# Kernel optimization log

Hardware: AMD Instinct MI355X
Metric: run time of the kernel (lower is better)

The kernel has to match this reference:

```python
import jax, jax.numpy as jnp
import numpy as np

N = 1200        # nodes in the (complete) graph
SLOPE = 0.1     # leaky_relu negative slope
# smat: 10-vector -> symmetric 4x4
SMAT_IDX = np.array([0,1,2,3,1,4,5,6,2,5,7,8,3,6,8,9])

def _glorot(k, shape):
    lim = float(np.sqrt(6.0 / (shape[0] + shape[1])))
    return jax.random.uniform(k, shape, jnp.float32, -lim, lim)

def setup_inputs():
    key = jax.random.key(0)
    ks = jax.random.split(key, 24)
    # complete graph connectivity (recover_S reads edge_map[i,j] for all i!=j)
    iu, ju = np.triu_indices(N, k=1)
    E = iu.shape[0]
    eid = np.arange(E, dtype=np.int32)
    edge_map = np.zeros((N, N), dtype=np.int32)
    edge_map[iu, ju] = eid
    edge_map[ju, iu] = eid
    ud_edges = np.stack([iu, ju], axis=1).astype(np.int32)           # [E,2]
    edge_index = np.stack([np.concatenate([iu, ju]),
                           np.concatenate([ju, iu])]).astype(np.int32)  # [2,2E]
    inp = {
        'x': jax.random.normal(ks[0], (N, 16), jnp.float32),
        'edge_index': jnp.asarray(edge_index),
        'edge_map': jnp.asarray(edge_map),
        'ud_edges': jnp.asarray(ud_edges),
    }
    dims = {'g': [(6, 32), (32, 32), (32, 64)],
            'n': [(64, 64), (64, 64), (64, 10)],
            'e': [(64, 64), (64, 64), (64, 16)]}
    k = 1
    for tag, ds in dims.items():
        for i, (a, b) in enumerate(ds):
            inp[f'W{tag}{i+1}'] = _glorot(ks[k], (a, b)); k += 1
            inp[f'b{tag}{i+1}'] = jnp.zeros((b,), jnp.float32)
    return inp

def _leaky(v):
    return jnp.where(v >= 0, v, SLOPE * v)

def _gcn(x, src, dst, W, b):
    deg = jax.ops.segment_sum(jnp.ones(src.shape[0], x.dtype), dst, num_segments=N)
    dinv = jnp.where(deg > 0, jax.lax.rsqrt(deg), 0.0)
    norm = dinv[src] * dinv[dst]
    h = x @ W
    return jax.ops.segment_sum(norm[:, None] * h[src], dst, num_segments=N) + b

def _mlp3(h, W1, b1, W2, b2, W3, b3):
    # dropout is identity (eval mode)
    h = _leaky(h @ W1 + b1)
    h = _leaky(h @ W2 + b2)
    return h @ W3 + b3

def _forward(x, edge_index, edge_map, ud_edges,
             Wg1, bg1, Wg2, bg2, Wg3, bg3,
             Wn1, bn1, Wn2, bn2, Wn3, bn3,
             We1, be1, We2, be2, We3, be3):
    x6 = x[:, 0:6]                       # node_feature_mode == 1
    src, dst = edge_index[0], edge_index[1]
    h = _leaky(_gcn(x6, src, dst, Wg1, bg1))
    h = _leaky(_gcn(h, src, dst, Wg2, bg2))
    h = _gcn(h, src, dst, Wg3, bg3)      # [N,64]
    vd = _mlp3(h, Wn1, bn1, Wn2, bn2, Wn3, bn3)            # [N,10]
    he = h[ud_edges[:, 0]] + h[ud_edges[:, 1]]             # [E,64]
    ed = _mlp3(he, We1, be1, We2, be2, We3, be3)           # [E,16]
    # recover_S: block-structured [4N,4N]
    Vsym = vd[:, jnp.asarray(SMAT_IDX)].reshape(N, 4, 4)   # smat per node
    Eb = ed.reshape(-1, 4, 4)
    B = Eb[edge_map]                                       # [N,N,4,4]
    ii = jnp.arange(N)
    lower = ii[:, None] > ii[None, :]
    B = jnp.where(lower[:, :, None, None], jnp.swapaxes(B, 2, 3), B)
    B = B.at[ii, ii].set(Vsym)
    S = B.transpose(0, 2, 1, 3).reshape(4 * N, 4 * N)
    return h, S

def reference(x, edge_index, edge_map, ud_edges,
              Wg1, bg1, Wg2, bg2, Wg3, bg3,
              Wn1, bn1, Wn2, bn2, Wn3, bn3,
              We1, be1, We2, be2, We3, be3):
    return _forward(x, edge_index, edge_map, ud_edges,
                    Wg1, bg1, Wg2, bg2, Wg3, bg3,
                    Wn1, bn1, Wn2, bn2, Wn3, bn3,
                    We1, be1, We2, be2, We3, be3)
```

## Files before the change

kernel.cpp:

```cpp
#include <hip/hip_runtime.h>

#define NN 1200
#define NE 719400
#define SDIM 4800

typedef __attribute__((ext_vector_type(8))) short bf16x8;
typedef __attribute__((ext_vector_type(4))) short bf16x4;
typedef __attribute__((ext_vector_type(4))) float f32x4;

static __device__ __constant__ int SMAT[16] = {0,1,2,3,1,4,5,6,2,5,7,8,3,6,8,9};

__device__ __forceinline__ float lk(float v) { return v >= 0.f ? v : 0.1f * v; }

#if __has_builtin(__builtin_amdgcn_mfma_f32_16x16x16bf16_1k)
__device__ __forceinline__ f32x4 mfma1616(bf16x4 a, bf16x4 b, f32x4 c) {
    return __builtin_amdgcn_mfma_f32_16x16x16bf16_1k(a, b, c, 0, 0, 0);
}
#else
__device__ __forceinline__ f32x4 mfma1616(bf16x4 a, bf16x4 b, f32x4 c) {
    asm volatile("v_mfma_f32_16x16x16_bf16 %0, %1, %2, %0\n\ts_nop 7\n\ts_nop 7"
                 : "+v"(c) : "v"(a), "v"(b));
    return c;
}
#endif

__device__ __forceinline__ void split8(const float* u, bf16x8& hi, bf16x8& lo) {
#pragma unroll
    for (int e = 0; e < 8; e++) {
        unsigned x = __float_as_uint(u[e]);
        unsigned r = x + 0x7FFFu + ((x >> 16) & 1u);
        hi[e] = (short)(r >> 16);
        float hf = __uint_as_float(r & 0xFFFF0000u);
        float s = u[e] - hf;
        unsigned v = __float_as_uint(s);
        unsigned w = v + 0x7FFFu + ((v >> 16) & 1u);
        lo[e] = (short)(w >> 16);
    }
}

__device__ __forceinline__ void split4(const float* u, bf16x4& hi, bf16x4& lo) {
#pragma unroll
    for (int e = 0; e < 4; e++) {
        unsigned x = __float_as_uint(u[e]);
        unsigned r = x + 0x7FFFu + ((x >> 16) & 1u);
        hi[e] = (short)(r >> 16);
        float hf = __uint_as_float(r & 0xFFFF0000u);
        float s = u[e] - hf;
        unsigned v = __float_as_uint(s);
        unsigned w = v + 0x7FFFu + ((v >> 16) & 1u);
        lo[e] = (short)(w >> 16);
    }
}

__device__ __forceinline__ uint2 split2(float a0, float a1) {
    unsigned u0 = __float_as_uint(a0), u1 = __float_as_uint(a1);
    unsigned r0 = u0 + 0x7FFFu + ((u0 >> 16) & 1u);
    unsigned r1 = u1 + 0x7FFFu + ((u1 >> 16) & 1u);
    float h0 = __uint_as_float(r0 & 0xFFFF0000u);
    float h1 = __uint_as_float(r1 & 0xFFFF0000u);
    float s0 = a0 - h0, s1 = a1 - h1;
    unsigned v0 = __float_as_uint(s0), v1 = __float_as_uint(s1);
    unsigned t0 = v0 + 0x7FFFu + ((v0 >> 16) & 1u);
    unsigned t1 = v1 + 0x7FFFu + ((v1 >> 16) & 1u);
    unsigned hi = (r0 >> 16) | (r1 & 0xFFFF0000u);
    unsigned lo = (t0 >> 16) | (t1 & 0xFFFF0000u);
    return make_uint2(hi, lo);
}

__global__ void k_prep(const float* __restrict__ We2, const float* __restrict__ We3,
                       unsigned* __restrict__ W2F, unsigned* __restrict__ W3F,
                       float* __restrict__ cs) {
    int t = blockIdx.x * 256 + threadIdx.x;
    if (t < 512) {
        int lane = t & 63, ks = (t >> 6) & 1, mt = t >> 7;
        int m = mt * 16 + (lane & 15);
        int kb = ks * 32 + (lane >> 4) * 8;
        unsigned hi[4], lo[4];
#pragma unroll
        for (int p = 0; p < 4; p++) {
            float a0 = We2[(kb + 2 * p) * 64 + m];
            float a1 = We2[(kb + 2 * p + 1) * 64 + m];
            uint2 hl = split2(a0, a1);
            hi[p] = hl.x; lo[p] = hl.y;
        }
        *(uint4*)(W2F + ((mt * 2 + ks) * 2 + 0) * 256 + lane * 4) = make_uint4(hi[0], hi[1], hi[2], hi[3]);
        *(uint4*)(W2F + ((mt * 2 + ks) * 2 + 1) * 256 + lane * 4) = make_uint4(lo[0], lo[1], lo[2], lo[3]);
    } else if (t < 768) {
        int q = t - 512;
        int lane = q & 63, kb = q >> 6;
        int c = lane & 15;
        int k0 = kb * 16 + (lane >> 4) * 4;
        unsigned hi[2], lo[2];
#pragma unroll
        for (int p = 0; p < 2; p++) {
            float a0 = We3[(k0 + 2 * p) * 16 + c];
            float a1 = We3[(k0 + 2 * p + 1) * 16 + c];
            uint2 hl = split2(a0, a1);
            hi[p] = hl.x; lo[p] = hl.y;
        }
        *(uint2*)(W3F + (kb * 2 + 0) * 128 + lane * 2) = make_uint2(hi[0], hi[1]);
        *(uint2*)(W3F + (kb * 2 + 1) * 128 + lane * 2) = make_uint2(lo[0], lo[1]);
    } else if (t < 896) {
        cs[t - 768] = 0.f;
    }
}

__global__ __launch_bounds__(256) void k_t1(const float* __restrict__ x,
                                            const float* __restrict__ Wg1,
                                            float* __restrict__ t1,
                                            float* __restrict__ cs1) {
    int T = blockIdx.x * 256 + threadIdx.x;
    int c = T & 31, rs = T >> 5;
    float w[6];
#pragma unroll
    for (int k = 0; k < 6; k++) w[k] = Wg1[k * 32 + c];
    float loc = 0.f;
    for (int r = rs; r < NN; r += 304) {
        float acc = 0.f;
#pragma unroll
        for (int k = 0; k < 6; k++) acc = fmaf(x[r * 16 + k], w[k], acc);
        t1[r * 32 + c] = acc;
        loc += acc;
    }
    atomicAdd(&cs1[c], loc);
}

__global__ __launch_bounds__(256) void k_t2(const float* __restrict__ t1,
                                            const float* __restrict__ cs1,
                                            const float* __restrict__ bg1,
                                            const float* __restrict__ Wg2,
                                            float* __restrict__ t2,
                                            float* __restrict__ cs2) {
    int T = blockIdx.x * 256 + threadIdx.x;
    int c = T & 31, rs = T >> 5;
    const float inv = 1.0f / 1199.0f;
    float p[32], w[32];
#pragma unroll
    for (int k = 0; k < 32; k++) {
        p[k] = fmaf(cs1[k], inv, bg1[k]);
        w[k] = Wg2[k * 32 + c];
    }
    float loc = 0.f;
    for (int r = rs; r < NN; r += 304) {
        float acc = 0.f;
#pragma unroll
        for (int k = 0; k < 32; k++) {
            float h = lk(fmaf(-t1[r * 32 + k], inv, p[k]));
            acc = fmaf(h, w[k], acc);
        }
        t2[r * 32 + c] = acc;
        loc += acc;
    }
    atomicAdd(&cs2[c], loc);
}

__global__ __launch_bounds__(256) void k_t3(const float* __restrict__ t2,
                                            const float* __restrict__ cs2,
                                            const float* __restrict__ bg2,
                                            const float* __restrict__ Wg3,
                                            float* __restrict__ t3,
                                            float* __restrict__ cs3) {
    int T = blockIdx.x * 256 + threadIdx.x;
    int c = T & 63, rs = T >> 6;
    const float inv = 1.0f / 1199.0f;
    float p[32], w[32];
#pragma unroll
    for (int k = 0; k < 32; k++) {
        p[k] = fmaf(cs2[k], inv, bg2[k]);
        w[k] = Wg3[k * 64 + c];
    }
    float loc = 0.f;
    for (int r = rs; r < NN; r += 152) {
        float acc = 0.f;
#pragma unroll
        for (int k = 0; k < 32; k++) {
            float h = lk(fmaf(-t2[r * 32 + k], inv, p[k]));
            acc = fmaf(h, w[k], acc);
        }
        t3[r * 64 + c] = acc;
        loc += acc;
    }
    atomicAdd(&cs3[c], loc);
}

__global__ __launch_bounds__(256) void k_g(const float* __restrict__ t3,
                                           const float* __restrict__ cs3,
                                           const float* __restrict__ bg3,
                                           const float* __restrict__ We1,
                                           float* __restrict__ h_out,
                                           float* __restrict__ g_out) {
    __shared__ float H[32][65];
    __shared__ float W[4096];
    const int tid = threadIdx.x;
    const int r0 = blockIdx.x * 32;
    const float inv = 1.0f / 1199.0f;

    for (int t = tid; t < 1024; t += 256) ((float4*)W)[t] = ((const float4*)We1)[t];
    for (int t = tid; t < 2048; t += 256) {
        int i = t >> 6, c = t & 63;
        int row = r0 + i;
        float v = 0.f;
        if (row < NN) {
            v = fmaf(cs3[c] - t3[row * 64 + c], inv, bg3[c]);
            h_out[row * 64 + c] = v;
        }
        H[i][c] = v;
    }
    __syncthreads();

    int rg = tid >> 3, cg = tid & 7;
    float acc[8] = {};
#pragma unroll 8
    for (int k = 0; k < 64; k++) {
        float a = H[rg][k];
        float4 b0 = *(const float4*)&W[k * 64 + cg * 8];
        float4 b1 = *(const float4*)&W[k * 64 + cg * 8 + 4];
        acc[0] = fmaf(a, b0.x, acc[0]); acc[1] = fmaf(a, b0.y, acc[1]);
        acc[2] = fmaf(a, b0.z, acc[2]); acc[3] = fmaf(a, b0.w, acc[3]);
        acc[4] = fmaf(a, b1.x, acc[4]); acc[5] = fmaf(a, b1.y, acc[5]);
        acc[6] = fmaf(a, b1.z, acc[6]); acc[7] = fmaf(a, b1.w, acc[7]);
    }
    int row = r0 + rg;
    if (row < NN) {
        *(float4*)&g_out[row * 64 + cg * 8]     = make_float4(acc[0], acc[1], acc[2], acc[3]);
        *(float4*)&g_out[row * 64 + cg * 8 + 4] = make_float4(acc[4], acc[5], acc[6], acc[7]);
    }
}

__global__ __launch_bounds__(256) void k_vd(const float* __restrict__ h,
                                            const float* __restrict__ Wn1, const float* __restrict__ bn1,
                                            const float* __restrict__ Wn2, const float* __restrict__ bn2,
                                            const float* __restrict__ Wn3, const float* __restrict__ bn3,
                                            float* __restrict__ S) {
    __shared__ float H[32][65];
    __shared__ float N1[32][65];
    __shared__ float WB[4096];
    __shared__ float WC[4096];
    __shared__ float WD[640];
    __shared__ float VD[32][12];
    __shared__ float sb1[64], sb2[64], sb3[16];

    const int tid = threadIdx.x;
    const int r0 = blockIdx.x * 32;

    for (int t = tid; t < 1024; t += 256) {
        ((float4*)WB)[t] = ((const float4*)Wn1)[t];
        ((float4*)WC)[t] = ((const float4*)Wn2)[t];
    }
    for (int t = tid; t < 640; t += 256) WD[t] = Wn3[t];
    if (tid < 64) { sb1[tid] = bn1[tid]; sb2[tid] = bn2[tid]; }
    if (tid < 10) sb3[tid] = bn3[tid];

    for (int t = tid; t < 2048; t += 256) {
        int i = t >> 6, c = t & 63;
        int row = r0 + i;
        H[i][c] = (row < NN) ? h[row * 64 + c] : 0.f;
    }
    __syncthreads();

    int rg = tid >> 3, cg = tid & 7;
    {
        float acc[8] = {};
#pragma unroll 8
        for (int k = 0; k < 64; k++) {
            float a = H[rg][k];
            float4 b0 = *(const float4*)&WB[k * 64 + cg * 8];
            float4 b1 = *(const float4*)&WB[k * 64 + cg * 8 + 4];
            acc[0] = fmaf(a, b0.x, acc[0]); acc[1] = fmaf(a, b0.y, acc[1]);
            acc[2] = fmaf(a, b0.z, acc[2]); acc[3] = fmaf(a, b0.w, acc[3]);
            acc[4] = fmaf(a, b1.x, acc[4]); acc[5] = fmaf(a, b1.y, acc[5]);
            acc[6] = fmaf(a, b1.z, acc[6]); acc[7] = fmaf(a, b1.w, acc[7]);
        }
#pragma unroll
        for (int q = 0; q < 8; q++) N1[rg][cg * 8 + q] = lk(acc[q] + sb1[cg * 8 + q]);
    }
    __syncthreads();
    {
        float acc[8] = {};
#pragma unroll 8
        for (int k = 0; k < 64; k++) {
            float a = N1[rg][k];
            float4 b0 = *(const float4*)&WC[k * 64 + cg * 8];
            float4 b1 = *(const float4*)&WC[k * 64 + cg * 8 + 4];
            acc[0] = fmaf(a, b0.x, acc[0]); acc[1] = fmaf(a, b0.y, acc[1]);
            acc[2] = fmaf(a, b0.z, acc[2]); acc[3] = fmaf(a, b0.w, acc[3]);
            acc[4] = fmaf(a, b1.x, acc[4]); acc[5] = fmaf(a, b1.y, acc[5]);
            acc[6] = fmaf(a, b1.z, acc[6]); acc[7] = fmaf(a, b1.w, acc[7]);
        }
#pragma unroll
        for (int q = 0; q < 8; q++) H[rg][cg * 8 + q] = lk(acc[q] + sb2[cg * 8 + q]);
    }
    __syncthreads();
    for (int t = tid; t < 320; t += 256) {
        int r = t / 10, c = t % 10;
        float acc = sb3[c];
        for (int k = 0; k < 64; k++) acc = fmaf(H[r][k], WD[k * 10 + c], acc);
        VD[r][c] = acc;
    }
    __syncthreads();
    if (tid < 128) {
        int r = tid >> 2, a = tid & 3;
        int row = r0 + r;
        if (row < NN) {
            float4 v = make_float4(VD[r][SMAT[a * 4 + 0]], VD[r][SMAT[a * 4 + 1]],
                                   VD[r][SMAT[a * 4 + 2]], VD[r][SMAT[a * 4 + 3]]);
            *(float4*)&S[(4 * row + a) * SDIM + 4 * row] = v;
        }
    }
}

__global__ __launch_bounds__(256) void k_edge(const int* __restrict__ ud,
                                              const float* __restrict__ g,
                                              const float* __restrict__ be1,
                                              const float* __restrict__ be2,
                                              const float* __restrict__ be3,
                                              const unsigned* __restrict__ W2F,
                                              const unsigned* __restrict__ W3F,
                                              float* __restrict__ S) {
    __shared__ float EDW[4][32][17];

    const int tid = threadIdx.x;
    const int wave = tid >> 6, lane = tid & 63;
    const int lrow = lane & 15, lgrp = lane >> 4;
    const int base_e = blockIdx.x * 128 + wave * 32;

    const int e0 = base_e + lrow;
    const int e1 = base_e + 16 + lrow;
    const int2 ij0 = ((const int2*)ud)[min(e0, NE - 1)];
    const int2 ij1 = ((const int2*)ud)[min(e1, NE - 1)];

    f32x4 b1a[2][2];
#pragma unroll
    for (int ks = 0; ks < 2; ks++) {
        b1a[ks][0] = *(const f32x4*)(be1 + ks * 32 + lgrp * 8);
        b1a[ks][1] = *(const f32x4*)(be1 + ks * 32 + lgrp * 8 + 4);
    }

    bf16x8 Uhi[2][2], Ulo[2][2];
#pragma unroll
    for (int nt = 0; nt < 2; nt++) {
        const int2 ij = nt ? ij1 : ij0;
        const float* gi = g + ij.x * 64;
        const float* gj = g + ij.y * 64;
#pragma unroll
        for (int ks = 0; ks < 2; ks++) {
            int kb = ks * 32 + lgrp * 8;
            f32x4 x0 = *(const f32x4*)(gi + kb);
            f32x4 x1 = *(const f32x4*)(gi + kb + 4);
            f32x4 y0 = *(const f32x4*)(gj + kb);
            f32x4 y1 = *(const f32x4*)(gj + kb + 4);
            float u[8];
#pragma unroll
            for (int e = 0; e < 4; e++) {
                u[e]     = lk(x0[e] + y0[e] + b1a[ks][0][e]);
                u[4 + e] = lk(x1[e] + y1[e] + b1a[ks][1][e]);
            }
            split8(u, Uhi[nt][ks], Ulo[nt][ks]);
        }
    }

    bf16x4 Vhi[4][2], Vlo[4][2];
#pragma unroll
    for (int mt = 0; mt < 4; mt++) {
        f32x4 acc[2];
#pragma unroll
        for (int nt = 0; nt < 2; nt++)
#pragma unroll
            for (int q = 0; q < 4; q++) acc[nt][q] = 0.f;
#pragma unroll
        for (int ks = 0; ks < 2; ks++) {
            bf16x8 Whi = *(const bf16x8*)(W2F + ((mt * 2 + ks) * 2 + 0) * 256 + lane * 4);
            bf16x8 Wlo = *(const bf16x8*)(W2F + ((mt * 2 + ks) * 2 + 1) * 256 + lane * 4);
#pragma unroll
            for (int nt = 0; nt < 2; nt++) {
                acc[nt] = __builtin_amdgcn_mfma_f32_16x16x32_bf16(Whi, Uhi[nt][ks], acc[nt], 0, 0, 0);
                acc[nt] = __builtin_amdgcn_mfma_f32_16x16x32_bf16(Wlo, Uhi[nt][ks], acc[nt], 0, 0, 0);
                acc[nt] = __builtin_amdgcn_mfma_f32_16x16x32_bf16(Whi, Ulo[nt][ks], acc[nt], 0, 0, 0);
            }
        }
        f32x4 b2 = *(const f32x4*)(be2 + mt * 16 + lgrp * 4);
#pragma unroll
        for (int nt = 0; nt < 2; nt++) {
            float v[4];
#pragma unroll
            for (int q = 0; q < 4; q++) v[q] = lk(acc[nt][q] + b2[q]);
            split4(v, Vhi[mt][nt], Vlo[mt][nt]);
        }
    }

    f32x4 acc3[2];
#pragma unroll
    for (int nt = 0; nt < 2; nt++)
#pragma unroll
        for (int q = 0; q < 4; q++) acc3[nt][q] = 0.f;
#pragma unroll
    for (int kb = 0; kb < 4; kb++) {
        bf16x4 W3h = *(const bf16x4*)(W3F + (kb * 2 + 0) * 128 + lane * 2);
        bf16x4 W3l = *(const bf16x4*)(W3F + (kb * 2 + 1) * 128 + lane * 2);
#pragma unroll
        for (int nt = 0; nt < 2; nt++) {
            acc3[nt] = mfma1616(W3h, Vhi[kb][nt], acc3[nt]);
            acc3[nt] = mfma1616(W3l, Vhi[kb][nt], acc3[nt]);
            acc3[nt] = mfma1616(W3h, Vlo[kb][nt], acc3[nt]);
        }
    }

    f32x4 b3 = *(const f32x4*)(be3 + lgrp * 4);
#pragma unroll
    for (int nt = 0; nt < 2; nt++) {
        const int e = nt ? e1 : e0;
        const int2 ij = nt ? ij1 : ij0;
        float ed[4];
#pragma unroll
        for (int q = 0; q < 4; q++) {
            ed[q] = acc3[nt][q] + b3[q];
            EDW[wave][nt * 16 + lrow][lgrp * 4 + q] = ed[q];
        }
        if (e < NE) {
            *(float4*)&S[(4 * ij.x + lgrp) * SDIM + 4 * ij.y] =
                make_float4(ed[0], ed[1], ed[2], ed[3]);
        }
    }

    const int le = lane & 31;
    const int lg2 = lane >> 5;
    const int eL = base_e + le;
    const int2 ijL = ((const int2*)ud)[min(eL, NE - 1)];
#pragma unroll
    for (int q = 0; q < 2; q++) {
        int a = lg2 * 2 + q;
        float4 v = make_float4(EDW[wave][le][a], EDW[wave][le][4 + a],
                               EDW[wave][le][8 + a], EDW[wave][le][12 + a]);
        if (eL < NE) *(float4*)&S[(4 * ijL.y + a) * SDIM + 4 * ijL.x] = v;
    }
}

extern "C" void kernel_launch(void* const* d_in, const int* in_sizes, int n_in,
                              void* d_out, int out_size, void* d_ws, size_t ws_size,
                              hipStream_t stream) {
    const float* x   = (const float*)d_in[0];
    const int*   ud  = (const int*)d_in[3];
    const float* Wg1 = (const float*)d_in[4];
    const float* bg1 = (const float*)d_in[5];
    const float* Wg2 = (const float*)d_in[6];
    const float* bg2 = (const float*)d_in[7];
    const float* Wg3 = (const float*)d_in[8];
    const float* bg3 = (const float*)d_in[9];
    const float* Wn1 = (const float*)d_in[10];
    const float* bn1 = (const float*)d_in[11];
    const float* Wn2 = (const float*)d_in[12];
    const float* bn2 = (const float*)d_in[13];
    const float* Wn3 = (const float*)d_in[14];
    const float* bn3 = (const float*)d_in[15];
    const float* We1 = (const float*)d_in[16];
    const float* be1 = (const float*)d_in[17];
    const float* We2 = (const float*)d_in[18];
    const float* be2 = (const float*)d_in[19];
    const float* We3 = (const float*)d_in[20];
    const float* be3 = (const float*)d_in[21];

    float* out   = (float*)d_out;
    float* h_out = out;
    float* S     = out + 76800;

    float* ws  = (float*)d_ws;
    float* t1  = ws;
    float* t2  = ws + 38400;
    float* t3  = ws + 76800;
    float* g   = ws + 153600;
    float* cs  = ws + 230400;
    unsigned* W2F = (unsigned*)(ws + 230528);
    unsigned* W3F = W2F + 4096;

    k_prep<<<4, 256, 0, stream>>>(We2, We3, W2F, W3F, cs);
    k_t1<<<38, 256, 0, stream>>>(x, Wg1, t1, cs);
    k_t2<<<38, 256, 0, stream>>>(t1, cs, bg1, Wg2, t2, cs + 32);
    k_t3<<<38, 256, 0, stream>>>(t2, cs + 32, bg2, Wg3, t3, cs + 64);
    k_g<<<38, 256, 0, stream>>>(t3, cs + 64, bg3, We1, h_out, g);
    k_edge<<<5621, 256, 0, stream>>>(ud, g, be1, be2, be3, W2F, W3F, S);
    k_vd<<<38, 256, 0, stream>>>(h_out, Wn1, bn1, Wn2, bn2, Wn3, bn3, S);
}
```

Measured before the change: 125.3 us.

## Fold weight prep and be1 into k_g, persistent edge kernel, hardware bf16 split

The k_prep kernel is removed. Its weight hi/lo splitting now runs in three extra blocks of k_g, and the cs zeroing becomes a hipMemsetAsync. The bias be1 is folded into g as 0.5*be1 per node, since he = g_i + g_j, which removes a per-edge bias load and add. The edge kernel becomes a grid-stride loop over tiles with 2048 blocks instead of 5621, and the bf16 hi/lo split uses the packed v_cvt_pk_bf16_f32 instruction instead of manual integer rounding. These aim to cut launch count and per-edge ALU work, at the risk of lower parallelism in the persistent edge loop.

```diff
diff --git a/kernel.cpp b/kernel.cpp
--- a/kernel.cpp
+++ b/kernel.cpp
@@ -3,6 +3,7 @@
 #define NN 1200
 #define NE 719400
 #define SDIM 4800
+#define NTILES 5621
 
 typedef __attribute__((ext_vector_type(8))) short bf16x8;
 typedef __attribute__((ext_vector_type(4))) short bf16x4;
@@ -24,85 +25,37 @@
 }
 #endif
 
+__device__ __forceinline__ unsigned cvtpk(float a0, float a1) {
+    unsigned r;
+    asm("v_cvt_pk_bf16_f32 %0, %1, %2" : "=v"(r) : "v"(a0), "v"(a1));
+    return r;
+}
+
+__device__ __forceinline__ void splitpk(float a0, float a1, unsigned& hw, unsigned& lw) {
+    hw = cvtpk(a0, a1);
+    float h0 = __uint_as_float(hw << 16);
+    float h1 = __uint_as_float(hw & 0xFFFF0000u);
+    lw = cvtpk(a0 - h0, a1 - h1);
+}
+
 __device__ __forceinline__ void split8(const float* u, bf16x8& hi, bf16x8& lo) {
-#pragma unroll
-    for (int e = 0; e < 8; e++) {
-        unsigned x = __float_as_uint(u[e]);
-        unsigned r = x + 0x7FFFu + ((x >> 16) & 1u);
-        hi[e] = (short)(r >> 16);
-        float hf = __uint_as_float(r & 0xFFFF0000u);
-        float s = u[e] - hf;
-        unsigned v = __float_as_uint(s);
-        unsigned w = v + 0x7FFFu + ((v >> 16) & 1u);
-        lo[e] = (short)(w >> 16);
-    }
+    union { unsigned w[4]; bf16x8 v; } H, L;
+#pragma unroll
+    for (int p = 0; p < 4; p++) splitpk(u[2 * p], u[2 * p + 1], H.w[p], L.w[p]);
+    hi = H.v; lo = L.v;
 }
 
 __device__ __forceinline__ void split4(const float* u, bf16x4& hi, bf16x4& lo) {
-#pragma unroll
-    for (int e = 0; e < 4; e++) {
-        unsigned x = __float_as_uint(u[e]);
-        unsigned r = x + 0x7FFFu + ((x >> 16) & 1u);
-        hi[e] = (short)(r >> 16);
-        float hf = __uint_as_float(r & 0xFFFF0000u);
-        float s = u[e] - hf;
-        unsigned v = __float_as_uint(s);
-        unsigned w = v + 0x7FFFu + ((v >> 16) & 1u);
-        lo[e] = (short)(w >> 16);
-    }
+    union { unsigned w[2]; bf16x4 v; } H, L;
+#pragma unroll
+    for (int p = 0; p < 2; p++) splitpk(u[2 * p], u[2 * p + 1], H.w[p], L.w[p]);
+    hi = H.v; lo = L.v;
 }
 
 __device__ __forceinline__ uint2 split2(float a0, float a1) {
-    unsigned u0 = __float_as_uint(a0), u1 = __float_as_uint(a1);
-    unsigned r0 = u0 + 0x7FFFu + ((u0 >> 16) & 1u);
-    unsigned r1 = u1 + 0x7FFFu + ((u1 >> 16) & 1u);
-    float h0 = __uint_as_float(r0 & 0xFFFF0000u);
-    float h1 = __uint_as_float(r1 & 0xFFFF0000u);
-    float s0 = a0 - h0, s1 = a1 - h1;
-    unsigned v0 = __float_as_uint(s0), v1 = __float_as_uint(s1);
-    unsigned t0 = v0 + 0x7FFFu + ((v0 >> 16) & 1u);
-    unsigned t1 = v1 + 0x7FFFu + ((v1 >> 16) & 1u);
-    unsigned hi = (r0 >> 16) | (r1 & 0xFFFF0000u);
-    unsigned lo = (t0 >> 16) | (t1 & 0xFFFF0000u);
-    return make_uint2(hi, lo);
-}
-
-__global__ void k_prep(const float* __restrict__ We2, const float* __restrict__ We3,
-                       unsigned* __restrict__ W2F, unsigned* __restrict__ W3F,
-                       float* __restrict__ cs) {
-    int t = blockIdx.x * 256 + threadIdx.x;
-    if (t < 512) {
-        int lane = t & 63, ks = (t >> 6) & 1, mt = t >> 7;
-        int m = mt * 16 + (lane & 15);
-        int kb = ks * 32 + (lane >> 4) * 8;
-        unsigned hi[4], lo[4];
-#pragma unroll
-        for (int p = 0; p < 4; p++) {
-            float a0 = We2[(kb + 2 * p) * 64 + m];
-            float a1 = We2[(kb + 2 * p + 1) * 64 + m];
-            uint2 hl = split2(a0, a1);
-            hi[p] = hl.x; lo[p] = hl.y;
-        }
-        *(uint4*)(W2F + ((mt * 2 + ks) * 2 + 0) * 256 + lane * 4) = make_uint4(hi[0], hi[1], hi[2], hi[3]);
-        *(uint4*)(W2F + ((mt * 2 + ks) * 2 + 1) * 256 + lane * 4) = make_uint4(lo[0], lo[1], lo[2], lo[3]);
-    } else if (t < 768) {
-        int q = t - 512;
-        int lane = q & 63, kb = q >> 6;
-        int c = lane & 15;
-        int k0 = kb * 16 + (lane >> 4) * 4;
-        unsigned hi[2], lo[2];
-#pragma unroll
-        for (int p = 0; p < 2; p++) {
-            float a0 = We3[(k0 + 2 * p) * 16 + c];
-            float a1 = We3[(k0 + 2 * p + 1) * 16 + c];
-            uint2 hl = split2(a0, a1);
-            hi[p] = hl.x; lo[p] = hl.y;
-        }
-        *(uint2*)(W3F + (kb * 2 + 0) * 128 + lane * 2) = make_uint2(hi[0], hi[1]);
-        *(uint2*)(W3F + (kb * 2 + 1) * 128 + lane * 2) = make_uint2(lo[0], lo[1]);
-    } else if (t < 896) {
-        cs[t - 768] = 0.f;
-    }
+    unsigned hw, lw;
+    splitpk(a0, a1, hw, lw);
+    return make_uint2(hw, lw);
 }
 
 __global__ __launch_bounds__(256) void k_t1(const float* __restrict__ x,
@@ -187,11 +140,47 @@
                                            const float* __restrict__ cs3,
                                            const float* __restrict__ bg3,
                                            const float* __restrict__ We1,
+                                           const float* __restrict__ be1,
+                                           const float* __restrict__ We2,
+                                           const float* __restrict__ We3,
                                            float* __restrict__ h_out,
-                                           float* __restrict__ g_out) {
+                                           float* __restrict__ g_out,
+                                           unsigned* __restrict__ W2F,
+                                           unsigned* __restrict__ W3F) {
+    const int tid = threadIdx.x;
+    if (blockIdx.x >= 38) {
+        int t = (blockIdx.x - 38) * 256 + tid;
+        if (t < 512) {
+            int lane = t & 63, ks = (t >> 6) & 1, mt = t >> 7;
+            int m = mt * 16 + (lane & 15);
+            int kb = ks * 32 + (lane >> 4) * 8;
+            unsigned hi[4], lo[4];
+#pragma unroll
+            for (int p = 0; p < 4; p++) {
+                uint2 hl = split2(We2[(kb + 2 * p) * 64 + m], We2[(kb + 2 * p + 1) * 64 + m]);
+                hi[p] = hl.x; lo[p] = hl.y;
+            }
+            *(uint4*)(W2F + ((mt * 2 + ks) * 2 + 0) * 256 + lane * 4) = make_uint4(hi[0], hi[1], hi[2], hi[3]);
+            *(uint4*)(W2F + ((mt * 2 + ks) * 2 + 1) * 256 + lane * 4) = make_uint4(lo[0], lo[1], lo[2], lo[3]);
+        } else if (t < 768) {
+            int q = t - 512;
+            int lane = q & 63, kb = q >> 6;
+            int c = lane & 15;
+            int k0 = kb * 16 + (lane >> 4) * 4;
+            unsigned hi[2], lo[2];
+#pragma unroll
+            for (int p = 0; p < 2; p++) {
+                uint2 hl = split2(We3[(k0 + 2 * p) * 16 + c], We3[(k0 + 2 * p + 1) * 16 + c]);
+                hi[p] = hl.x; lo[p] = hl.y;
+            }
+            *(uint2*)(W3F + (kb * 2 + 0) * 128 + lane * 2) = make_uint2(hi[0], hi[1]);
+            *(uint2*)(W3F + (kb * 2 + 1) * 128 + lane * 2) = make_uint2(lo[0], lo[1]);
+        }
+        return;
+    }
+
     __shared__ float H[32][65];
     __shared__ float W[4096];
-    const int tid = threadIdx.x;
     const int r0 = blockIdx.x * 32;
     const float inv = 1.0f / 1199.0f;
 
@@ -209,7 +198,9 @@
     __syncthreads();
 
     int rg = tid >> 3, cg = tid & 7;
-    float acc[8] = {};
+    float acc[8];
+#pragma unroll
+    for (int q = 0; q < 8; q++) acc[q] = 0.5f * be1[cg * 8 + q];
 #pragma unroll 8
     for (int k = 0; k < 64; k++) {
         float a = H[rg][k];
@@ -311,7 +302,6 @@
 
 __global__ __launch_bounds__(256) void k_edge(const int* __restrict__ ud,
                                               const float* __restrict__ g,
-                                              const float* __restrict__ be1,
                                               const float* __restrict__ be2,
                                               const float* __restrict__ be3,
                                               const unsigned* __restrict__ W2F,
@@ -322,116 +312,110 @@
     const int tid = threadIdx.x;
     const int wave = tid >> 6, lane = tid & 63;
     const int lrow = lane & 15, lgrp = lane >> 4;
-    const int base_e = blockIdx.x * 128 + wave * 32;
-
-    const int e0 = base_e + lrow;
-    const int e1 = base_e + 16 + lrow;
-    const int2 ij0 = ((const int2*)ud)[min(e0, NE - 1)];
-    const int2 ij1 = ((const int2*)ud)[min(e1, NE - 1)];
-
-    f32x4 b1a[2][2];
-#pragma unroll
-    for (int ks = 0; ks < 2; ks++) {
-        b1a[ks][0] = *(const f32x4*)(be1 + ks * 32 + lgrp * 8);
-        b1a[ks][1] = *(const f32x4*)(be1 + ks * 32 + lgrp * 8 + 4);
-    }
-
-    bf16x8 Uhi[2][2], Ulo[2][2];
-#pragma unroll
-    for (int nt = 0; nt < 2; nt++) {
-        const int2 ij = nt ? ij1 : ij0;
-        const float* gi = g + ij.x * 64;
-        const float* gj = g + ij.y * 64;
-#pragma unroll
-        for (int ks = 0; ks < 2; ks++) {
-            int kb = ks * 32 + lgrp * 8;
-            f32x4 x0 = *(const f32x4*)(gi + kb);
-            f32x4 x1 = *(const f32x4*)(gi + kb + 4);
-            f32x4 y0 = *(const f32x4*)(gj + kb);
-            f32x4 y1 = *(const f32x4*)(gj + kb + 4);
-            float u[8];
-#pragma unroll
-            for (int e = 0; e < 4; e++) {
-                u[e]     = lk(x0[e] + y0[e] + b1a[ks][0][e]);
-                u[4 + e] = lk(x1[e] + y1[e] + b1a[ks][1][e]);
-            }
-            split8(u, Uhi[nt][ks], Ulo[nt][ks]);
-        }
-    }
-
-    bf16x4 Vhi[4][2], Vlo[4][2];
-#pragma unroll
-    for (int mt = 0; mt < 4; mt++) {
-        f32x4 acc[2];
+    const int le = lane & 31, lg2 = lane >> 5;
+
+    for (int tile = blockIdx.x; tile < NTILES; tile += gridDim.x) {
+        const int base_e = tile * 128 + wave * 32;
+        const int e0 = base_e + lrow;
+        const int e1 = base_e + 16 + lrow;
+        const int2 ij0 = ((const int2*)ud)[min(e0, NE - 1)];
+        const int2 ij1 = ((const int2*)ud)[min(e1, NE - 1)];
+
+        bf16x8 Uhi[2][2], Ulo[2][2];
+#pragma unroll
+        for (int nt = 0; nt < 2; nt++) {
+            const int2 ij = nt ? ij1 : ij0;
+            const float* gi = g + ij.x * 64;
+            const float* gj = g + ij.y * 64;
+#pragma unroll
+            for (int ks = 0; ks < 2; ks++) {
+                int kb = ks * 32 + lgrp * 8;
+                f32x4 x0 = *(const f32x4*)(gi + kb);
+                f32x4 x1 = *(const f32x4*)(gi + kb + 4);
+                f32x4 y0 = *(const f32x4*)(gj + kb);
+                f32x4 y1 = *(const f32x4*)(gj + kb + 4);
+                float u[8];
+#pragma unroll
+                for (int e = 0; e < 4; e++) {
+                    u[e]     = lk(x0[e] + y0[e]);
+                    u[4 + e] = lk(x1[e] + y1[e]);
+                }
+                split8(u, Uhi[nt][ks], Ulo[nt][ks]);
+            }
+        }
+
+        bf16x4 Vhi[4][2], Vlo[4][2];
+#pragma unroll
+        for (int mt = 0; mt < 4; mt++) {
+            f32x4 acc[2];
+#pragma unroll
+            for (int nt = 0; nt < 2; nt++)
+#pragma unroll
+                for (int q = 0; q < 4; q++) acc[nt][q] = 0.f;
+#pragma unroll
+            for (int ks = 0; ks < 2; ks++) {
+                bf16x8 Whi = *(const bf16x8*)(W2F + ((mt * 2 + ks) * 2 + 0) * 256 + lane * 4);
+                bf16x8 Wlo = *(const bf16x8*)(W2F + ((mt * 2 + ks) * 2 + 1) * 256 + lane * 4);
+#pragma unroll
+                for (int nt = 0; nt < 2; nt++) {
+                    acc[nt] = __builtin_amdgcn_mfma_f32_16x16x32_bf16(Whi, Uhi[nt][ks], acc[nt], 0, 0, 0);
+                    acc[nt] = __builtin_amdgcn_mfma_f32_16x16x32_bf16(Wlo, Uhi[nt][ks], acc[nt], 0, 0, 0);
+                    acc[nt] = __builtin_amdgcn_mfma_f32_16x16x32_bf16(Whi, Ulo[nt][ks], acc[nt], 0, 0, 0);
+                }
+            }
+            f32x4 b2 = *(const f32x4*)(be2 + mt * 16 + lgrp * 4);
+#pragma unroll
+            for (int nt = 0; nt < 2; nt++) {
+                float v[4];
+#pragma unroll
+                for (int q = 0; q < 4; q++) v[q] = lk(acc[nt][q] + b2[q]);
+                split4(v, Vhi[mt][nt], Vlo[mt][nt]);
+            }
+        }
+
+        f32x4 acc3[2];
 #pragma unroll
         for (int nt = 0; nt < 2; nt++)
 #pragma unroll
-            for (int q = 0; q < 4; q++) acc[nt][q] = 0.f;
-#pragma unroll
-        for (int ks = 0; ks < 2; ks++) {
-            bf16x8 Whi = *(const bf16x8*)(W2F + ((mt * 2 + ks) * 2 + 0) * 256 + lane * 4);
-            bf16x8 Wlo = *(const bf16x8*)(W2F + ((mt * 2 + ks) * 2 + 1) * 256 + lane * 4);
+            for (int q = 0; q < 4; q++) acc3[nt][q] = 0.f;
+#pragma unroll
+        for (int kb = 0; kb < 4; kb++) {
+            bf16x4 W3h = *(const bf16x4*)(W3F + (kb * 2 + 0) * 128 + lane * 2);
+            bf16x4 W3l = *(const bf16x4*)(W3F + (kb * 2 + 1) * 128 + lane * 2);
 #pragma unroll
             for (int nt = 0; nt < 2; nt++) {
-                acc[nt] = __builtin_amdgcn_mfma_f32_16x16x32_bf16(Whi, Uhi[nt][ks], acc[nt], 0, 0, 0);
-                acc[nt] = __builtin_amdgcn_mfma_f32_16x16x32_bf16(Wlo, Uhi[nt][ks], acc[nt], 0, 0, 0);
-                acc[nt] = __builtin_amdgcn_mfma_f32_16x16x32_bf16(Whi, Ulo[nt][ks], acc[nt], 0, 0, 0);
-            }
-        }
-        f32x4 b2 = *(const f32x4*)(be2 + mt * 16 + lgrp * 4);
+                acc3[nt] = mfma1616(W3h, Vhi[kb][nt], acc3[nt]);
+                acc3[nt] = mfma1616(W3l, Vhi[kb][nt], acc3[nt]);
+                acc3[nt] = mfma1616(W3h, Vlo[kb][nt], acc3[nt]);
+            }
+        }
+
+        f32x4 b3 = *(const f32x4*)(be3 + lgrp * 4);
 #pragma unroll
         for (int nt = 0; nt < 2; nt++) {
-            float v[4];
-#pragma unroll
-            for (int q = 0; q < 4; q++) v[q] = lk(acc[nt][q] + b2[q]);
-            split4(v, Vhi[mt][nt], Vlo[mt][nt]);
-        }
-    }
-
-    f32x4 acc3[2];
-#pragma unroll
-    for (int nt = 0; nt < 2; nt++)
-#pragma unroll
-        for (int q = 0; q < 4; q++) acc3[nt][q] = 0.f;
-#pragma unroll
-    for (int kb = 0; kb < 4; kb++) {
-        bf16x4 W3h = *(const bf16x4*)(W3F + (kb * 2 + 0) * 128 + lane * 2);
-        bf16x4 W3l = *(const bf16x4*)(W3F + (kb * 2 + 1) * 128 + lane * 2);
-#pragma unroll
-        for (int nt = 0; nt < 2; nt++) {
-            acc3[nt] = mfma1616(W3h, Vhi[kb][nt], acc3[nt]);
-            acc3[nt] = mfma1616(W3l, Vhi[kb][nt], acc3[nt]);
-            acc3[nt] = mfma1616(W3h, Vlo[kb][nt], acc3[nt]);
-        }
-    }
-
-    f32x4 b3 = *(const f32x4*)(be3 + lgrp * 4);
-#pragma unroll
-    for (int nt = 0; nt < 2; nt++) {
-        const int e = nt ? e1 : e0;
-        const int2 ij = nt ? ij1 : ij0;
-        float ed[4];
-#pragma unroll
-        for (int q = 0; q < 4; q++) {
-            ed[q] = acc3[nt][q] + b3[q];
-            EDW[wave][nt * 16 + lrow][lgrp * 4 + q] = ed[q];
-        }
-        if (e < NE) {
-            *(float4*)&S[(4 * ij.x + lgrp) * SDIM + 4 * ij.y] =
-                make_float4(ed[0], ed[1], ed[2], ed[3]);
-        }
-    }
-
-    const int le = lane & 31;
-    const int lg2 = lane >> 5;
-    const int eL = base_e + le;
-    const int2 ijL = ((const int2*)ud)[min(eL, NE - 1)];
-#pragma unroll
-    for (int q = 0; q < 2; q++) {
-        int a = lg2 * 2 + q;
-        float4 v = make_float4(EDW[wave][le][a], EDW[wave][le][4 + a],
-                               EDW[wave][le][8 + a], EDW[wave][le][12 + a]);
-        if (eL < NE) *(float4*)&S[(4 * ijL.y + a) * SDIM + 4 * ijL.x] = v;
+            const int e = nt ? e1 : e0;
+            const int2 ij = nt ? ij1 : ij0;
+            float ed[4];
+#pragma unroll
+            for (int q = 0; q < 4; q++) {
+                ed[q] = acc3[nt][q] + b3[q];
+                EDW[wave][nt * 16 + lrow][lgrp * 4 + q] = ed[q];
+            }
+            if (e < NE) {
+                *(float4*)&S[(4 * ij.x + lgrp) * SDIM + 4 * ij.y] =
+                    make_float4(ed[0], ed[1], ed[2], ed[3]);
+            }
+        }
+
+        const int eL = base_e + le;
+        const int2 ijL = ((const int2*)ud)[min(eL, NE - 1)];
+#pragma unroll
+        for (int q = 0; q < 2; q++) {
+            int a = lg2 * 2 + q;
+            float4 v = make_float4(EDW[wave][le][a], EDW[wave][le][4 + a],
+                                   EDW[wave][le][8 + a], EDW[wave][le][12 + a]);
+            if (eL < NE) *(float4*)&S[(4 * ijL.y + a) * SDIM + 4 * ijL.x] = v;
+        }
     }
 }
 
@@ -472,11 +456,11 @@
     unsigned* W2F = (unsigned*)(ws + 230528);
     unsigned* W3F = W2F + 4096;
 
-    k_prep<<<4, 256, 0, stream>>>(We2, We3, W2F, W3F, cs);
+    hipMemsetAsync(cs, 0, 128 * sizeof(float), stream);
     k_t1<<<38, 256, 0, stream>>>(x, Wg1, t1, cs);
     k_t2<<<38, 256, 0, stream>>>(t1, cs, bg1, Wg2, t2, cs + 32);
     k_t3<<<38, 256, 0, stream>>>(t2, cs + 32, bg2, Wg3, t3, cs + 64);
-    k_g<<<38, 256, 0, stream>>>(t3, cs + 64, bg3, We1, h_out, g);
-    k_edge<<<5621, 256, 0, stream>>>(ud, g, be1, be2, be3, W2F, W3F, S);
+    k_g<<<41, 256, 0, stream>>>(t3, cs + 64, bg3, We1, be1, We2, We3, h_out, g, W2F, W3F);
+    k_edge<<<2048, 256, 0, stream>>>(ud, g, be2, be3, W2F, W3F, S);
     k_vd<<<38, 256, 0, stream>>>(h_out, Wn1, bn1, Wn2, bn2, Wn3, bn3, S);
 }
```

New measurement: 133.2 us. 6.3% more time.
